# Kernel optimization log

Hardware: AMD Instinct MI355X
Metric: run time of the kernel (lower is better)

Reference implementation:

```python
import jax, jax.numpy as jnp
import numpy as np

N_HEADS = 16


def _rope(x, sin, cos):
    # x: [B, H, T, D]; sin/cos: [1, 1, T, D]
    x1 = x[..., ::2]
    x2 = x[..., 1::2]
    xr = jnp.stack((-x2, x1), axis=-1).reshape(x.shape)
    return x * cos + xr * sin


def setup_inputs() -> dict:
    key = jax.random.key(0)
    k_x, k_s, k_c, k_w1, k_w2 = jax.random.split(key, 5)
    B, T, C = 4, 2048, 2048
    hd = C // N_HEADS
    x = jax.random.normal(k_x, (B, T, C), dtype=jnp.float32)
    sin = jax.random.uniform(k_s, (1, 1, T, hd), dtype=jnp.float32)
    cos = jax.random.uniform(k_c, (1, 1, T, hd), dtype=jnp.float32)
    W_qkv = jax.random.normal(k_w1, (C, 3 * C), dtype=jnp.float32) * 0.02
    W_proj = jax.random.normal(k_w2, (C, C), dtype=jnp.float32) * 0.02
    return {"x": x, "sin": sin, "cos": cos, "W_qkv": W_qkv, "W_proj": W_proj}


def reference(x, sin, cos, W_qkv, W_proj):
    B, T, C = x.shape
    hd = C // N_HEADS
    qkv = x @ W_qkv  # [B, T, 3C]
    q, k, v = jnp.split(qkv, 3, axis=-1)
    # [B, T, C] -> [B, H, T, D]
    q = q.reshape(B, T, N_HEADS, hd).transpose(0, 2, 1, 3)
    k = k.reshape(B, T, N_HEADS, hd).transpose(0, 2, 1, 3)
    v = v.reshape(B, T, N_HEADS, hd).transpose(0, 2, 1, 3)
    q = _rope(q, sin[:, :, :T, :], cos[:, :, :T, :])
    k = _rope(k, sin[:, :, :T, :], cos[:, :, :T, :])
    scale = 1.0 / jnp.sqrt(jnp.asarray(hd, dtype=x.dtype))
    scores = jnp.einsum("bhqd,bhkd->bhqk", q, k) * scale
    causal = jnp.tril(jnp.ones((T, T), dtype=bool))
    scores = jnp.where(causal, scores, jnp.asarray(-jnp.inf, dtype=scores.dtype))
    attn = jax.nn.softmax(scores, axis=-1)
    y = jnp.einsum("bhqk,bhkd->bhqd", attn, v)  # [B, H, T, D]
    y = y.transpose(0, 2, 1, 3).reshape(B, T, C)
    return y @ W_proj
```

## Files before the change

kernel.cpp:

```cpp
#include <hip/hip_runtime.h>
#include <hip/hip_bf16.h>
#include <stdint.h>

typedef uint32_t u32;
typedef uint16_t u16;
typedef __attribute__((ext_vector_type(8))) short short8;
typedef __attribute__((ext_vector_type(4))) float floatx4;

#define NH 16
#define HD 128
#define TSEQ 2048
#define NB 4
#define CM 2048
#define MROWS (NB*TSEQ)
#define NQKV (3*CM)

__device__ __forceinline__ u16 f2bf(float f) {
    union { float f; u32 u; } v; v.f = f;
    return (u16)((v.u + 0x7fffu + ((v.u >> 16) & 1u)) >> 16);
}

__global__ __launch_bounds__(256) void convert_x_kernel(const float* __restrict__ in,
                                                        u16* __restrict__ out) {
    int idx = (blockIdx.x * 256 + threadIdx.x) * 8;
    float4 a = *(const float4*)(in + idx);
    float4 b = *(const float4*)(in + idx + 4);
    union { u16 s[8]; uint4 v; } o;
    o.s[0] = f2bf(a.x); o.s[1] = f2bf(a.y); o.s[2] = f2bf(a.z); o.s[3] = f2bf(a.w);
    o.s[4] = f2bf(b.x); o.s[5] = f2bf(b.y); o.s[6] = f2bf(b.z); o.s[7] = f2bf(b.w);
    *(uint4*)(out + idx) = o.v;
}

__global__ __launch_bounds__(256) void transpose_bf_kernel(const float* __restrict__ in,
                                                           u16* __restrict__ out,
                                                           int R, int Cn) {
    __shared__ float tile[32][33];
    int tx = threadIdx.x, ty = threadIdx.y;
    int c0 = blockIdx.x * 32, r0 = blockIdx.y * 32;
#pragma unroll
    for (int i = 0; i < 4; i++)
        tile[ty + i * 8][tx] = in[(size_t)(r0 + ty + i * 8) * Cn + c0 + tx];
    __syncthreads();
#pragma unroll
    for (int i = 0; i < 4; i++)
        out[(size_t)(c0 + ty + i * 8) * R + r0 + tx] = f2bf(tile[tx][ty + i * 8]);
}

__global__ __launch_bounds__(256, 2) void gemm_qkv_rope(const u16* __restrict__ A,
                                                        const u16* __restrict__ BT,
                                                        const float* __restrict__ sinp,
                                                        const float* __restrict__ cosp,
                                                        u16* __restrict__ q_ws,
                                                        u16* __restrict__ k_ws,
                                                        u16* __restrict__ v_ws) {
    __shared__ u16 As[128 * 40];
    __shared__ u16 Bs[128 * 40];
    int tid = threadIdx.x;
    int w = tid >> 6, lane = tid & 63, quad = lane >> 4, l15 = lane & 15;
    int mw = (w >> 1) * 64, nw = (w & 1) * 64;
    int blk = blockIdx.x;
    int xcd = blk & 7, idx8 = blk >> 3;
    int rowBase = (xcd * 8 + (idx8 & 7)) * 128;
    int colBase = (idx8 >> 3) * 128;

    floatx4 acc[4][4];
#pragma unroll
    for (int mi = 0; mi < 4; mi++)
#pragma unroll
        for (int ni = 0; ni < 4; ni++) acc[mi][ni] = (floatx4){0.f, 0.f, 0.f, 0.f};

    int r0s = tid >> 2, c8s = (tid & 3) * 8;
    int r1s = (tid + 256) >> 2;
    const u16* Arow0 = A + (size_t)(rowBase + r0s) * CM + c8s;
    const u16* Arow1 = A + (size_t)(rowBase + r1s) * CM + c8s;
    const u16* Brow0 = BT + (size_t)(colBase + r0s) * CM + c8s;
    const u16* Brow1 = BT + (size_t)(colBase + r1s) * CM + c8s;

    uint4 pa0 = *(const uint4*)(Arow0), pa1 = *(const uint4*)(Arow1);
    uint4 pb0 = *(const uint4*)(Brow0), pb1 = *(const uint4*)(Brow1);

    for (int k0 = 0; k0 < CM; k0 += 32) {
        __syncthreads();
        *(uint4*)(&As[r0s * 40 + c8s]) = pa0;
        *(uint4*)(&As[r1s * 40 + c8s]) = pa1;
        *(uint4*)(&Bs[r0s * 40 + c8s]) = pb0;
        *(uint4*)(&Bs[r1s * 40 + c8s]) = pb1;
        __syncthreads();
        if (k0 + 32 < CM) {
            pa0 = *(const uint4*)(Arow0 + k0 + 32);
            pa1 = *(const uint4*)(Arow1 + k0 + 32);
            pb0 = *(const uint4*)(Brow0 + k0 + 32);
            pb1 = *(const uint4*)(Brow1 + k0 + 32);
        }
        short8 af[4], bf[4];
#pragma unroll
        for (int mi = 0; mi < 4; mi++)
            af[mi] = *(const short8*)(&As[(mw + mi * 16 + l15) * 40 + quad * 8]);
#pragma unroll
        for (int ni = 0; ni < 4; ni++)
            bf[ni] = *(const short8*)(&Bs[(nw + ni * 16 + l15) * 40 + quad * 8]);
#pragma unroll
        for (int mi = 0; mi < 4; mi++)
#pragma unroll
            for (int ni = 0; ni < 4; ni++)
                acc[mi][ni] = __builtin_amdgcn_mfma_f32_16x16x32_bf16(af[mi], bf[ni],
                                                                      acc[mi][ni], 0, 0, 0);
    }

    const float inv_sqrt_hd = 0.08838834764831845f;
#pragma unroll
    for (int mi = 0; mi < 4; mi++) {
#pragma unroll
        for (int ni = 0; ni < 4; ni++) {
            int j = colBase + nw + ni * 16 + l15;
            int sec = j >> 11;
            int jj = j & 2047;
            int h = jj >> 7, d = jj & 127;
            if (sec == 2) {
                int r0 = rowBase + mw + mi * 16 + quad * 4;
                int b = r0 >> 11, t0 = r0 & 2047;
                union { u16 s[4]; uint2 v; } pk;
#pragma unroll
                for (int reg = 0; reg < 4; reg++) pk.s[reg] = f2bf(acc[mi][ni][reg]);
                *(uint2*)(&v_ws[((size_t)(b * NH + h) * HD + d) * TSEQ + t0]) = pk.v;
            } else {
#pragma unroll
                for (int reg = 0; reg < 4; reg++) {
                    int r = rowBase + mw + mi * 16 + quad * 4 + reg;
                    int b = r >> 11, t = r & 2047;
                    float v = acc[mi][ni][reg];
                    float partner = __shfl_xor(v, 1, 64);
                    size_t dsti = (size_t)((b * NH + h) * TSEQ + t) * HD + d;
                    float s = sinp[t * HD + d], c = cosp[t * HD + d];
                    float o = v * c + ((d & 1) ? partner * s : -partner * s);
                    if (sec == 0) o *= inv_sqrt_hd;
                    ((sec == 0) ? q_ws : k_ws)[dsti] = f2bf(o);
                }
            }
        }
    }
}

__global__ __launch_bounds__(256, 1) void attn_kernel(const u16* __restrict__ q_ws,
                                                      const u16* __restrict__ k_ws,
                                                      const u16* __restrict__ vt_ws,
                                                      u16* __restrict__ y_bf) {
    __shared__ u16 smem[16 * 1024];
    __shared__ u16 Ps[128 * 72];
    u16* Ks = smem;
    u16* Vt = smem + 8192;
    int tid = threadIdx.x;
    int w = tid >> 6, lane = tid & 63, quad = lane >> 4, l15 = lane & 15;
    int qt = 15 - (blockIdx.x >> 6);
    int bh = blockIdx.x & 63;
    int b = bh >> 4, h = bh & 15;
    const u16* Qg = q_ws + (size_t)bh * TSEQ * HD;
    const u16* Kg = k_ws + (size_t)bh * TSEQ * HD;
    const u16* Vg = vt_ws + (size_t)bh * HD * TSEQ;

    uint4 kreg[4], vreg[4];
#pragma unroll
    for (int j = 0; j < 4; j++) {
        int idx = j * 256 + tid;
        int key = idx >> 4, s = idx & 15;
        kreg[j] = *(const uint4*)(Kg + (size_t)key * HD + s * 8);
    }
#pragma unroll
    for (int j = 0; j < 4; j++) {
        int idx = j * 256 + tid;
        int d = idx >> 3, s = idx & 7;
        vreg[j] = *(const uint4*)(Vg + (size_t)d * TSEQ + s * 8);
    }

#pragma unroll
    for (int j = 0; j < 8; j++) {
        int idx = j * 256 + tid;
        int row = idx >> 4, s = idx & 15;
        uint4 qv = *(const uint4*)(Qg + (size_t)(qt * 128 + row) * HD + s * 8);
        *(uint4*)(&smem[s * 1024 + ((row ^ (s & 7)) * 8)]) = qv;
    }
    __syncthreads();
    short8 qf[2][4];
#pragma unroll
    for (int mi = 0; mi < 2; mi++)
#pragma unroll
        for (int kk = 0; kk < 4; kk++) {
            int row = w * 32 + mi * 16 + l15;
            int s = kk * 4 + quad;
            qf[mi][kk] = *(const short8*)(&smem[s * 1024 + ((row ^ (s & 7)) * 8)]);
        }

    floatx4 O[2][8];
#pragma unroll
    for (int mi = 0; mi < 2; mi++)
#pragma unroll
        for (int f = 0; f < 8; f++) O[mi][f] = (floatx4){0.f, 0.f, 0.f, 0.f};
    float l_i[2][4];
#pragma unroll
    for (int mi = 0; mi < 2; mi++)
#pragma unroll
        for (int g = 0; g < 4; g++) l_i[mi][g] = 0.f;

    int ktmax = 2 * qt + 1;
    for (int kt = 0; kt <= ktmax; kt++) {
        __syncthreads();
#pragma unroll
        for (int j = 0; j < 4; j++) {
            int idx = j * 256 + tid;
            int key = idx >> 4, s = idx & 15;
            *(uint4*)(&Ks[s * 512 + ((key ^ (s & 7)) * 8)]) = kreg[j];
        }
#pragma unroll
        for (int j = 0; j < 4; j++) {
            int idx = j * 256 + tid;
            int d = idx >> 3, s = idx & 7;
            *(uint4*)(&Vt[s * 1024 + ((d ^ s) * 8)]) = vreg[j];
        }
        __syncthreads();
        if (kt < ktmax) {
            const u16* Ktg = Kg + (size_t)((kt + 1) * 64) * HD;
            const u16* Vtg = Vg + (kt + 1) * 64;
#pragma unroll
            for (int j = 0; j < 4; j++) {
                int idx = j * 256 + tid;
                int key = idx >> 4, s = idx & 15;
                kreg[j] = *(const uint4*)(Ktg + (size_t)key * HD + s * 8);
            }
#pragma unroll
            for (int j = 0; j < 4; j++) {
                int idx = j * 256 + tid;
                int d = idx >> 3, s = idx & 7;
                vreg[j] = *(const uint4*)(Vtg + (size_t)d * TSEQ + s * 8);
            }
        }

        floatx4 S[2][4];
#pragma unroll
        for (int nf = 0; nf < 4; nf++) {
            short8 bb[4];
#pragma unroll
            for (int kk = 0; kk < 4; kk++) {
                int s = kk * 4 + quad;
                int key = nf * 16 + l15;
                bb[kk] = *(const short8*)(&Ks[s * 512 + ((key ^ (s & 7)) * 8)]);
            }
#pragma unroll
            for (int mi = 0; mi < 2; mi++) {
                floatx4 a4 = (floatx4){0.f, 0.f, 0.f, 0.f};
#pragma unroll
                for (int kk = 0; kk < 4; kk++)
                    a4 = __builtin_amdgcn_mfma_f32_16x16x32_bf16(qf[mi][kk], bb[kk], a4, 0, 0, 0);
                S[mi][nf] = a4;
            }
        }
        if (kt >= 2 * qt) {
#pragma unroll
            for (int mi = 0; mi < 2; mi++)
#pragma unroll
                for (int nf = 0; nf < 4; nf++) {
                    int key = kt * 64 + nf * 16 + l15;
#pragma unroll
                    for (int reg = 0; reg < 4; reg++) {
                        int query = qt * 128 + w * 32 + mi * 16 + quad * 4 + reg;
                        if (key > query) S[mi][nf][reg] = -1e4f;
                    }
                }
        }
#pragma unroll
        for (int mi = 0; mi < 2; mi++)
#pragma unroll
            for (int nf = 0; nf < 4; nf++)
#pragma unroll
                for (int reg = 0; reg < 4; reg++) {
                    float p = __expf(S[mi][nf][reg]);
                    l_i[mi][reg] += p;
                    Ps[(w * 32 + mi * 16 + quad * 4 + reg) * 72 + nf * 16 + l15] = f2bf(p);
                }
        short8 pa[2][2];
#pragma unroll
        for (int mi = 0; mi < 2; mi++)
#pragma unroll
            for (int kk = 0; kk < 2; kk++)
                pa[mi][kk] = *(const short8*)(&Ps[(w * 32 + mi * 16 + l15) * 72 +
                                                  kk * 32 + quad * 8]);
#pragma unroll
        for (int f = 0; f < 8; f++) {
            short8 vb[2];
#pragma unroll
            for (int kk = 0; kk < 2; kk++) {
                int s = kk * 4 + quad;
                int d = f * 16 + l15;
                vb[kk] = *(const short8*)(&Vt[s * 1024 + ((d ^ s) * 8)]);
            }
#pragma unroll
            for (int mi = 0; mi < 2; mi++)
#pragma unroll
                for (int kk = 0; kk < 2; kk++)
                    O[mi][f] = __builtin_amdgcn_mfma_f32_16x16x32_bf16(pa[mi][kk], vb[kk],
                                                                       O[mi][f], 0, 0, 0);
        }
    }

    float inv[2][4];
#pragma unroll
    for (int mi = 0; mi < 2; mi++)
#pragma unroll
        for (int reg = 0; reg < 4; reg++) {
            float l = l_i[mi][reg];
#pragma unroll
            for (int off = 1; off < 16; off <<= 1) l += __shfl_xor(l, off, 64);
            inv[mi][reg] = 1.0f / l;
        }
#pragma unroll
    for (int mi = 0; mi < 2; mi++)
#pragma unroll
        for (int f = 0; f < 8; f++)
#pragma unroll
            for (int reg = 0; reg < 4; reg++) {
                int t = qt * 128 + w * 32 + mi * 16 + quad * 4 + reg;
                int col = h * HD + f * 16 + l15;
                y_bf[(size_t)(b * TSEQ + t) * CM + col] = f2bf(O[mi][f][reg] * inv[mi][reg]);
            }
}

__global__ __launch_bounds__(256, 2) void gemm_proj(const u16* __restrict__ A,
                                                    const u16* __restrict__ BT,
                                                    float* __restrict__ out) {
    __shared__ u16 As[128 * 40];
    __shared__ u16 Bs[128 * 40];
    int tid = threadIdx.x;
    int w = tid >> 6, lane = tid & 63, quad = lane >> 4, l15 = lane & 15;
    int mw = (w >> 1) * 64, nw = (w & 1) * 64;
    int blk = blockIdx.x;
    int xcd = blk & 7, idx8 = blk >> 3;
    int rowBase = (xcd * 8 + (idx8 & 7)) * 128;
    int colBase = (idx8 >> 3) * 128;

    floatx4 acc[4][4];
#pragma unroll
    for (int mi = 0; mi < 4; mi++)
#pragma unroll
        for (int ni = 0; ni < 4; ni++) acc[mi][ni] = (floatx4){0.f, 0.f, 0.f, 0.f};

    int r0s = tid >> 2, c8s = (tid & 3) * 8;
    int r1s = (tid + 256) >> 2;
    const u16* Arow0 = A + (size_t)(rowBase + r0s) * CM + c8s;
    const u16* Arow1 = A + (size_t)(rowBase + r1s) * CM + c8s;
    const u16* Brow0 = BT + (size_t)(colBase + r0s) * CM + c8s;
    const u16* Brow1 = BT + (size_t)(colBase + r1s) * CM + c8s;

    uint4 pa0 = *(const uint4*)(Arow0), pa1 = *(const uint4*)(Arow1);
    uint4 pb0 = *(const uint4*)(Brow0), pb1 = *(const uint4*)(Brow1);

    for (int k0 = 0; k0 < CM; k0 += 32) {
        __syncthreads();
        *(uint4*)(&As[r0s * 40 + c8s]) = pa0;
        *(uint4*)(&As[r1s * 40 + c8s]) = pa1;
        *(uint4*)(&Bs[r0s * 40 + c8s]) = pb0;
        *(uint4*)(&Bs[r1s * 40 + c8s]) = pb1;
        __syncthreads();
        if (k0 + 32 < CM) {
            pa0 = *(const uint4*)(Arow0 + k0 + 32);
            pa1 = *(const uint4*)(Arow1 + k0 + 32);
            pb0 = *(const uint4*)(Brow0 + k0 + 32);
            pb1 = *(const uint4*)(Brow1 + k0 + 32);
        }
        short8 af[4], bf[4];
#pragma unroll
        for (int mi = 0; mi < 4; mi++)
            af[mi] = *(const short8*)(&As[(mw + mi * 16 + l15) * 40 + quad * 8]);
#pragma unroll
        for (int ni = 0; ni < 4; ni++)
            bf[ni] = *(const short8*)(&Bs[(nw + ni * 16 + l15) * 40 + quad * 8]);
#pragma unroll
        for (int mi = 0; mi < 4; mi++)
#pragma unroll
            for (int ni = 0; ni < 4; ni++)
                acc[mi][ni] = __builtin_amdgcn_mfma_f32_16x16x32_bf16(af[mi], bf[ni],
                                                                      acc[mi][ni], 0, 0, 0);
    }

#pragma unroll
    for (int mi = 0; mi < 4; mi++) {
#pragma unroll
        for (int ni = 0; ni < 4; ni++) {
            int j = colBase + nw + ni * 16 + l15;
#pragma unroll
            for (int reg = 0; reg < 4; reg++) {
                int r = rowBase + mw + mi * 16 + quad * 4 + reg;
                out[(size_t)r * CM + j] = acc[mi][ni][reg];
            }
        }
    }
}

extern "C" void kernel_launch(void* const* d_in, const int* in_sizes, int n_in,
                              void* d_out, int out_size, void* d_ws, size_t ws_size,
                              hipStream_t stream) {
    const float* x      = (const float*)d_in[0];
    const float* sinp   = (const float*)d_in[1];
    const float* cosp   = (const float*)d_in[2];
    const float* W_qkv  = (const float*)d_in[3];
    const float* W_proj = (const float*)d_in[4];
    float* out = (float*)d_out;

    char* ws = (char*)d_ws;
    size_t off = 0;
    u16* x_bf   = (u16*)(ws + off); off += (size_t)MROWS * CM * 2;
    u16* wqkvT  = (u16*)(ws + off); off += (size_t)NQKV * CM * 2;
    u16* wprojT = (u16*)(ws + off); off += (size_t)CM * CM * 2;
    u16* q_ws   = (u16*)(ws + off); off += (size_t)MROWS * CM * 2;
    u16* k_ws   = (u16*)(ws + off); off += (size_t)MROWS * CM * 2;
    u16* v_ws   = (u16*)(ws + off); off += (size_t)MROWS * CM * 2;
    u16* y_bf   = x_bf;

    convert_x_kernel<<<(MROWS * CM) / (256 * 8), 256, 0, stream>>>(x, x_bf);
    transpose_bf_kernel<<<dim3(NQKV / 32, CM / 32), dim3(32, 8), 0, stream>>>(W_qkv, wqkvT, CM, NQKV);
    transpose_bf_kernel<<<dim3(CM / 32, CM / 32), dim3(32, 8), 0, stream>>>(W_proj, wprojT, CM, CM);
    gemm_qkv_rope<<<(NQKV / 128) * (MROWS / 128), 256, 0, stream>>>(x_bf, wqkvT, sinp, cosp,
                                                                    q_ws, k_ws, v_ws);
    attn_kernel<<<(TSEQ / 128) * 64, 256, 0, stream>>>(q_ws, k_ws, v_ws, y_bf);
    gemm_proj<<<(CM / 128) * (MROWS / 128), 256, 0, stream>>>(y_bf, wprojT, out);
}
```

Measured before the change: 751.3 us.

## Use 512-thread attention blocks with one 16-row query slice per wave

The attention kernel goes from 4 waves each owning 32 query rows to 8 waves each owning 16 rows of the 128-row query tile. Global-to-LDS K/V staging is spread over twice as many threads, so each thread holds half the prefetch registers and half the accumulators. This aims to raise wave-level parallelism and latency hiding per CU. In exchange, each K/V fragment read from LDS is reused by only one MFMA row block instead of two, so LDS read traffic per unit of compute doubles.

Result: faster. 734.0 us (-2.3%).

```diff
diff --git a/kernel.cpp b/kernel.cpp
--- a/kernel.cpp
+++ b/kernel.cpp
@@ -141,7 +141,7 @@
     }
 }
 
-__global__ __launch_bounds__(256, 1) void attn_kernel(const u16* __restrict__ q_ws,
+__global__ __launch_bounds__(512, 1) void attn_kernel(const u16* __restrict__ q_ws,
                                                       const u16* __restrict__ k_ws,
                                                       const u16* __restrict__ vt_ws,
                                                       u16* __restrict__ y_bf) {
@@ -158,61 +158,55 @@
     const u16* Kg = k_ws + (size_t)bh * TSEQ * HD;
     const u16* Vg = vt_ws + (size_t)bh * HD * TSEQ;
 
-    uint4 kreg[4], vreg[4];
-#pragma unroll
-    for (int j = 0; j < 4; j++) {
-        int idx = j * 256 + tid;
+    uint4 kreg[2], vreg[2];
+#pragma unroll
+    for (int j = 0; j < 2; j++) {
+        int idx = j * 512 + tid;
         int key = idx >> 4, s = idx & 15;
         kreg[j] = *(const uint4*)(Kg + (size_t)key * HD + s * 8);
     }
 #pragma unroll
-    for (int j = 0; j < 4; j++) {
-        int idx = j * 256 + tid;
+    for (int j = 0; j < 2; j++) {
+        int idx = j * 512 + tid;
         int d = idx >> 3, s = idx & 7;
         vreg[j] = *(const uint4*)(Vg + (size_t)d * TSEQ + s * 8);
     }
 
 #pragma unroll
-    for (int j = 0; j < 8; j++) {
-        int idx = j * 256 + tid;
+    for (int j = 0; j < 4; j++) {
+        int idx = j * 512 + tid;
         int row = idx >> 4, s = idx & 15;
         uint4 qv = *(const uint4*)(Qg + (size_t)(qt * 128 + row) * HD + s * 8);
         *(uint4*)(&smem[s * 1024 + ((row ^ (s & 7)) * 8)]) = qv;
     }
     __syncthreads();
-    short8 qf[2][4];
-#pragma unroll
-    for (int mi = 0; mi < 2; mi++)
-#pragma unroll
-        for (int kk = 0; kk < 4; kk++) {
-            int row = w * 32 + mi * 16 + l15;
-            int s = kk * 4 + quad;
-            qf[mi][kk] = *(const short8*)(&smem[s * 1024 + ((row ^ (s & 7)) * 8)]);
-        }
-
-    floatx4 O[2][8];
-#pragma unroll
-    for (int mi = 0; mi < 2; mi++)
-#pragma unroll
-        for (int f = 0; f < 8; f++) O[mi][f] = (floatx4){0.f, 0.f, 0.f, 0.f};
-    float l_i[2][4];
-#pragma unroll
-    for (int mi = 0; mi < 2; mi++)
-#pragma unroll
-        for (int g = 0; g < 4; g++) l_i[mi][g] = 0.f;
+    short8 qf[4];
+#pragma unroll
+    for (int kk = 0; kk < 4; kk++) {
+        int row = w * 16 + l15;
+        int s = kk * 4 + quad;
+        qf[kk] = *(const short8*)(&smem[s * 1024 + ((row ^ (s & 7)) * 8)]);
+    }
+
+    floatx4 O[8];
+#pragma unroll
+    for (int f = 0; f < 8; f++) O[f] = (floatx4){0.f, 0.f, 0.f, 0.f};
+    float l_i[4];
+#pragma unroll
+    for (int g = 0; g < 4; g++) l_i[g] = 0.f;
 
     int ktmax = 2 * qt + 1;
     for (int kt = 0; kt <= ktmax; kt++) {
         __syncthreads();
 #pragma unroll
-        for (int j = 0; j < 4; j++) {
-            int idx = j * 256 + tid;
+        for (int j = 0; j < 2; j++) {
+            int idx = j * 512 + tid;
             int key = idx >> 4, s = idx & 15;
             *(uint4*)(&Ks[s * 512 + ((key ^ (s & 7)) * 8)]) = kreg[j];
         }
 #pragma unroll
-        for (int j = 0; j < 4; j++) {
-            int idx = j * 256 + tid;
+        for (int j = 0; j < 2; j++) {
+            int idx = j * 512 + tid;
             int d = idx >> 3, s = idx & 7;
             *(uint4*)(&Vt[s * 1024 + ((d ^ s) * 8)]) = vreg[j];
         }
@@ -221,20 +215,20 @@
             const u16* Ktg = Kg + (size_t)((kt + 1) * 64) * HD;
             const u16* Vtg = Vg + (kt + 1) * 64;
 #pragma unroll
-            for (int j = 0; j < 4; j++) {
-                int idx = j * 256 + tid;
+            for (int j = 0; j < 2; j++) {
+                int idx = j * 512 + tid;
                 int key = idx >> 4, s = idx & 15;
                 kreg[j] = *(const uint4*)(Ktg + (size_t)key * HD + s * 8);
             }
 #pragma unroll
-            for (int j = 0; j < 4; j++) {
-                int idx = j * 256 + tid;
+            for (int j = 0; j < 2; j++) {
+                int idx = j * 512 + tid;
                 int d = idx >> 3, s = idx & 7;
                 vreg[j] = *(const uint4*)(Vtg + (size_t)d * TSEQ + s * 8);
             }
         }
 
-        floatx4 S[2][4];
+        floatx4 S[4];
 #pragma unroll
         for (int nf = 0; nf < 4; nf++) {
             short8 bb[4];
@@ -244,45 +238,35 @@
                 int key = nf * 16 + l15;
                 bb[kk] = *(const short8*)(&Ks[s * 512 + ((key ^ (s & 7)) * 8)]);
             }
-#pragma unroll
-            for (int mi = 0; mi < 2; mi++) {
-                floatx4 a4 = (floatx4){0.f, 0.f, 0.f, 0.f};
-#pragma unroll
-                for (int kk = 0; kk < 4; kk++)
-                    a4 = __builtin_amdgcn_mfma_f32_16x16x32_bf16(qf[mi][kk], bb[kk], a4, 0, 0, 0);
-                S[mi][nf] = a4;
-            }
+            floatx4 a4 = (floatx4){0.f, 0.f, 0.f, 0.f};
+#pragma unroll
+            for (int kk = 0; kk < 4; kk++)
+                a4 = __builtin_amdgcn_mfma_f32_16x16x32_bf16(qf[kk], bb[kk], a4, 0, 0, 0);
+            S[nf] = a4;
         }
         if (kt >= 2 * qt) {
 #pragma unroll
-            for (int mi = 0; mi < 2; mi++)
-#pragma unroll
-                for (int nf = 0; nf < 4; nf++) {
-                    int key = kt * 64 + nf * 16 + l15;
-#pragma unroll
-                    for (int reg = 0; reg < 4; reg++) {
-                        int query = qt * 128 + w * 32 + mi * 16 + quad * 4 + reg;
-                        if (key > query) S[mi][nf][reg] = -1e4f;
-                    }
+            for (int nf = 0; nf < 4; nf++) {
+                int key = kt * 64 + nf * 16 + l15;
+#pragma unroll
+                for (int reg = 0; reg < 4; reg++) {
+                    int query = qt * 128 + w * 16 + quad * 4 + reg;
+                    if (key > query) S[nf][reg] = -1e4f;
                 }
-        }
-#pragma unroll
-        for (int mi = 0; mi < 2; mi++)
-#pragma unroll
-            for (int nf = 0; nf < 4; nf++)
-#pragma unroll
-                for (int reg = 0; reg < 4; reg++) {
-                    float p = __expf(S[mi][nf][reg]);
-                    l_i[mi][reg] += p;
-                    Ps[(w * 32 + mi * 16 + quad * 4 + reg) * 72 + nf * 16 + l15] = f2bf(p);
-                }
-        short8 pa[2][2];
-#pragma unroll
-        for (int mi = 0; mi < 2; mi++)
-#pragma unroll
-            for (int kk = 0; kk < 2; kk++)
-                pa[mi][kk] = *(const short8*)(&Ps[(w * 32 + mi * 16 + l15) * 72 +
-                                                  kk * 32 + quad * 8]);
+            }
+        }
+#pragma unroll
+        for (int nf = 0; nf < 4; nf++)
+#pragma unroll
+            for (int reg = 0; reg < 4; reg++) {
+                float p = __expf(S[nf][reg]);
+                l_i[reg] += p;
+                Ps[(w * 16 + quad * 4 + reg) * 72 + nf * 16 + l15] = f2bf(p);
+            }
+        short8 pa[2];
+#pragma unroll
+        for (int kk = 0; kk < 2; kk++)
+            pa[kk] = *(const short8*)(&Ps[(w * 16 + l15) * 72 + kk * 32 + quad * 8]);
 #pragma unroll
         for (int f = 0; f < 8; f++) {
             short8 vb[2];
@@ -293,34 +277,27 @@
                 vb[kk] = *(const short8*)(&Vt[s * 1024 + ((d ^ s) * 8)]);
             }
 #pragma unroll
-            for (int mi = 0; mi < 2; mi++)
-#pragma unroll
-                for (int kk = 0; kk < 2; kk++)
-                    O[mi][f] = __builtin_amdgcn_mfma_f32_16x16x32_bf16(pa[mi][kk], vb[kk],
-                                                                       O[mi][f], 0, 0, 0);
-        }
-    }
-
-    float inv[2][4];
-#pragma unroll
-    for (int mi = 0; mi < 2; mi++)
+            for (int kk = 0; kk < 2; kk++)
+                O[f] = __builtin_amdgcn_mfma_f32_16x16x32_bf16(pa[kk], vb[kk], O[f], 0, 0, 0);
+        }
+    }
+
+    float inv[4];
+#pragma unroll
+    for (int reg = 0; reg < 4; reg++) {
+        float l = l_i[reg];
+#pragma unroll
+        for (int off = 1; off < 16; off <<= 1) l += __shfl_xor(l, off, 64);
+        inv[reg] = 1.0f / l;
+    }
+#pragma unroll
+    for (int f = 0; f < 8; f++)
 #pragma unroll
         for (int reg = 0; reg < 4; reg++) {
-            float l = l_i[mi][reg];
-#pragma unroll
-            for (int off = 1; off < 16; off <<= 1) l += __shfl_xor(l, off, 64);
-            inv[mi][reg] = 1.0f / l;
-        }
-#pragma unroll
-    for (int mi = 0; mi < 2; mi++)
-#pragma unroll
-        for (int f = 0; f < 8; f++)
-#pragma unroll
-            for (int reg = 0; reg < 4; reg++) {
-                int t = qt * 128 + w * 32 + mi * 16 + quad * 4 + reg;
-                int col = h * HD + f * 16 + l15;
-                y_bf[(size_t)(b * TSEQ + t) * CM + col] = f2bf(O[mi][f][reg] * inv[mi][reg]);
-            }
+            int t = qt * 128 + w * 16 + quad * 4 + reg;
+            int col = h * HD + f * 16 + l15;
+            y_bf[(size_t)(b * TSEQ + t) * CM + col] = f2bf(O[f][reg] * inv[reg]);
+        }
 }
 
 __global__ __launch_bounds__(256, 2) void gemm_proj(const u16* __restrict__ A,
@@ -419,6 +396,6 @@
     transpose_bf_kernel<<<dim3(CM / 32, CM / 32), dim3(32, 8), 0, stream>>>(W_proj, wprojT, CM, CM);
     gemm_qkv_rope<<<(NQKV / 128) * (MROWS / 128), 256, 0, stream>>>(x_bf, wqkvT, sinp, cosp,
                                                                     q_ws, k_ws, v_ws);
-    attn_kernel<<<(TSEQ / 128) * 64, 256, 0, stream>>>(q_ws, k_ws, v_ws, y_bf);
+    attn_kernel<<<(TSEQ / 128) * 64, 512, 0, stream>>>(q_ws, k_ws, v_ws, y_bf);
     gemm_proj<<<(CM / 128) * (MROWS / 128), 256, 0, stream>>>(y_bf, wprojT, out);
 }
```
